# Optimization experiments

Hardware: AMD Instinct MI355X
Metric: run time of the kernel (lower is better)

## Reference

```python
import jax, jax.numpy as jnp
import numpy as np

TEMPERATURE = 0.07
EPS = 1e-12  # F.normalize eps


def _construct_labels(visual_ids, anchor_idx):
    # Faithful vectorization of the original order-dependent double loop:
    # for i < B-1: final write to labels[i] comes from pair (i, B-1)
    #   -> 1 iff ids[i]==anchor_id and ids[B-1]==anchor_id, else 0
    # for i == B-1: final write comes from pair (B-2, B-1)
    #   -> 1 iff ids[B-1]==anchor_id and ids[B-2]==anchor_id, else 0
    B = visual_ids.shape[0]
    anchor_id = visual_ids[anchor_idx]
    same = visual_ids == anchor_id  # [B] bool
    labels = jnp.where(same & same[B - 1], 1, 0).astype(jnp.int32)
    labels = labels.at[B - 1].set((same[B - 1] & same[B - 2]).astype(jnp.int32))
    return labels


def setup_inputs() -> dict:
    key = jax.random.key(0)
    k1, k2 = jax.random.split(key)
    visual_feat = jax.random.normal(k1, (8192, 512), dtype=jnp.float32)
    visual_ids = jax.random.randint(k2, (8192,), 0, 1024, dtype=jnp.int64 if jax.config.jax_enable_x64 else jnp.int32)
    anchor_idx = 3
    return {"visual_feat": visual_feat, "visual_ids": visual_ids, "anchor_idx": anchor_idx}


def reference(visual_feat, visual_ids, anchor_idx):
    # L2 normalize rows (F.normalize: x / max(||x||, eps))
    norm = jnp.sqrt(jnp.sum(visual_feat * visual_feat, axis=1, keepdims=True))
    f = visual_feat / jnp.maximum(norm, EPS)
    sim = jnp.matmul(f, f.T) / TEMPERATURE  # [B, B]
    labels = _construct_labels(visual_ids, anchor_idx)  # [B] int in {0,1}
    logp = jax.nn.log_softmax(sim, axis=-1)  # [B, B]
    picked = jnp.take_along_axis(logp, labels[:, None], axis=1)[:, 0]
    loss = -jnp.mean(picked)
    return loss
```

## Files before the change

kernel.cpp:

```cpp
#include <hip/hip_runtime.h>


typedef int i32x8 __attribute__((ext_vector_type(8)));
typedef float f32x4 __attribute__((ext_vector_type(4)));

#define B_N 8192
#define D_K 512
#define ROWB 512
#define INVT 14.285714285714286f
#define SCALE_LOG2 20.609929155556622f

#if defined(__has_builtin) && __has_builtin(__builtin_amdgcn_exp2f)
#define FAST_EXP2(x) __builtin_amdgcn_exp2f(x)
#else
#define FAST_EXP2(x) exp2f(x)
#endif

union FragU {
  int4 h[2];
  i32x8 v;
};

static __device__ __forceinline__ void load16_to_lds(const void* g, void* l) {
  __builtin_amdgcn_global_load_lds(
      (const __attribute__((address_space(1))) unsigned int*)g,
      (__attribute__((address_space(3))) unsigned int*)l, 16, 0, 0);
}

__global__ __launch_bounds__(256)
void norm_kernel(const float* __restrict__ x,
                 unsigned char* __restrict__ fQ,
                 float* __restrict__ Z) {
  const int row = blockIdx.x * 4 + (threadIdx.x >> 6);
  const int lane = threadIdx.x & 63;
  const float4* xr = (const float4*)(x + (size_t)row * D_K);
  float4 a = xr[2 * lane];
  float4 b = xr[2 * lane + 1];
  float s = a.x * a.x + a.y * a.y + a.z * a.z + a.w * a.w +
            b.x * b.x + b.y * b.y + b.z * b.z + b.w * b.w;
#pragma unroll
  for (int off = 1; off < 64; off <<= 1) s += __shfl_xor(s, off);
  const float inv = 1.0f / fmaxf(sqrtf(s), 1e-12f);
  int lo = 0, hi = 0;
  lo = __builtin_amdgcn_cvt_pk_fp8_f32(a.x * inv, a.y * inv, lo, false);
  lo = __builtin_amdgcn_cvt_pk_fp8_f32(a.z * inv, a.w * inv, lo, true);
  hi = __builtin_amdgcn_cvt_pk_fp8_f32(b.x * inv, b.y * inv, hi, false);
  hi = __builtin_amdgcn_cvt_pk_fp8_f32(b.z * inv, b.w * inv, hi, true);
  int2 p; p.x = lo; p.y = hi;
  ((int2*)(fQ + (size_t)row * ROWB))[lane] = p;
  if (lane == 0) Z[row] = 0.0f;
}

__global__ __launch_bounds__(256, 2)
void sim_kernel(const unsigned char* __restrict__ fQ,
                float* __restrict__ Z, float* __restrict__ T01,
                float* __restrict__ D) {
  __shared__ unsigned char ldsA[4][128 * 128];
  __shared__ unsigned char ldsB[128 * 128];

  const int tid = threadIdx.x;
  const int lane = tid & 63;
  const int w = tid >> 6;
  const int wm = w & 1;
  const int wn = w >> 1;
  const int bx = blockIdx.x, by = blockIdx.y;
  const int b = by & 7;
  const int I = (by < 8) ? bx : (63 - bx);
  const int Jfirst = I + ((b - I) & 7);
  if (Jfirst > 63) return;
  const int I0 = I * 128;

  const int srow = lane >> 3;
  const int sb = lane & 7;
  const int su = sb ^ srow;
  const int sg = 2 * (su & 3) + (su >> 2);
  const size_t sOff = (size_t)srow * ROWB + sg * 16;

  const int fr = lane & 15;
  const int q = lane >> 4;
  const int swz = fr & 7;

  const int raRow = (wm * 64 + fr) * 128;
  const unsigned char* rbBase = ldsB + (wn * 64 + fr) * 128;
  const int off0 = (q ^ swz) * 16;
  const int off1 = ((q + 4) ^ swz) * 16;

#pragma unroll
  for (int kk = 0; kk < 4; ++kk) {
    const unsigned char* gA = fQ + (size_t)(I0 + w * 32) * ROWB + kk * 128 + sOff;
    unsigned char* lA = ldsA[kk] + (w * 32) * 128;
#pragma unroll
    for (int rr = 0; rr < 32; rr += 8)
      load16_to_lds(gA + (size_t)rr * ROWB, lA + rr * 128);
  }

  float Zp[4][4];
#pragma unroll
  for (int m = 0; m < 4; ++m)
#pragma unroll
    for (int r = 0; r < 4; ++r) Zp[m][r] = 0.0f;

#pragma unroll 1
  for (int J = Jfirst; J < 64; J += 8) {
    const int J0 = J * 128;
    f32x4 acc[4][4];
#pragma unroll
    for (int m = 0; m < 4; ++m)
#pragma unroll
      for (int n = 0; n < 4; ++n) acc[m][n] = (f32x4){0.f, 0.f, 0.f, 0.f};

#pragma unroll 1
    for (int kk = 0; kk < 4; ++kk) {
      const int k0 = kk * 128;
      {
        const unsigned char* gB = fQ + (size_t)(J0 + w * 32) * ROWB + k0 + sOff;
        unsigned char* lB = ldsB + (w * 32) * 128;
#pragma unroll
        for (int rr = 0; rr < 32; rr += 8)
          load16_to_lds(gB + (size_t)rr * ROWB, lB + rr * 128);
      }
      __syncthreads();

      const unsigned char* raBase = ldsA[kk] + raRow;
      i32x8 bv[4];
#pragma unroll
      for (int n = 0; n < 4; ++n) {
        const unsigned char* rb = rbBase + n * 16 * 128;
        FragU u;
        u.h[0] = *(const int4*)(rb + off0);
        u.h[1] = *(const int4*)(rb + off1);
        bv[n] = u.v;
      }
#pragma unroll
      for (int mh = 0; mh < 2; ++mh) {
        i32x8 av[2];
#pragma unroll
        for (int m = 0; m < 2; ++m) {
          const unsigned char* ra = raBase + (mh * 2 + m) * 16 * 128;
          FragU u;
          u.h[0] = *(const int4*)(ra + off0);
          u.h[1] = *(const int4*)(ra + off1);
          av[m] = u.v;
        }
#pragma unroll
        for (int m = 0; m < 2; ++m)
#pragma unroll
          for (int n = 0; n < 4; ++n)
            acc[mh * 2 + m][n] = __builtin_amdgcn_mfma_scale_f32_16x16x128_f8f6f4(
                av[m], bv[n], acc[mh * 2 + m][n], 0, 0, 0, 127, 0, 127);
      }
      __syncthreads();
    }

    if (I == 0 && wm == 0) {
      if (q == 0) {
#pragma unroll
        for (int n = 0; n < 4; ++n) {
          const int col = J0 + wn * 64 + n * 16 + fr;
          T01[col * 2 + 0] = acc[0][n][0] * INVT;
          T01[col * 2 + 1] = acc[0][n][1] * INVT;
        }
      }
    }

    if (J == I) {
#pragma unroll
      for (int m = 0; m < 4; ++m)
#pragma unroll
        for (int n = 0; n < 4; ++n) {
          const int col = J0 + wn * 64 + n * 16 + fr;
#pragma unroll
          for (int r = 0; r < 4; ++r) {
            const int row = I0 + wm * 64 + m * 16 + q * 4 + r;
            if (row == col) D[row] = acc[m][n][r];
          }
        }
    }

    const bool offd = (J != I);
#pragma unroll
    for (int n = 0; n < 4; ++n) {
      float cs = 0.0f;
#pragma unroll
      for (int m = 0; m < 4; ++m)
#pragma unroll
        for (int r = 0; r < 4; ++r) {
          const float e = FAST_EXP2((acc[m][n][r] - 1.0f) * SCALE_LOG2);
          Zp[m][r] += e;
          cs += e;
        }
      if (offd) {
        cs += __shfl_xor(cs, 16);
        cs += __shfl_xor(cs, 32);
        if (q == 0) atomicAdd(&Z[J0 + wn * 64 + n * 16 + fr], cs);
      }
    }
  }

#pragma unroll
  for (int m = 0; m < 4; ++m)
#pragma unroll
    for (int r = 0; r < 4; ++r) {
      float v = Zp[m][r];
      v += __shfl_xor(v, 1);
      v += __shfl_xor(v, 2);
      v += __shfl_xor(v, 4);
      v += __shfl_xor(v, 8);
      if (fr == 0) atomicAdd(&Z[I0 + wm * 64 + m * 16 + q * 4 + r], v);
    }
}

__global__ __launch_bounds__(1024)
void finalize_kernel(const float* __restrict__ Z,
                     const float* __restrict__ T01,
                     const float* __restrict__ D,
                     const int* __restrict__ ids,
                     const int* __restrict__ anchor,
                     float* __restrict__ out) {
  __shared__ float red[1024];
  const int t = threadIdx.x;
  const int anchor_id = ids[anchor[0]];
  const int sameLast = (ids[B_N - 1] == anchor_id);
  const int samePrev = (ids[B_N - 2] == anchor_id);
  int i[8], id[8];
  float z[8], d[8], t0[8], t1[8];
#pragma unroll
  for (int u = 0; u < 8; ++u) {
    i[u] = u * 1024 + t;
    z[u] = Z[i[u]];
    d[u] = D[i[u]];
    t0[u] = T01[i[u] * 2 + 0];
    t1[u] = T01[i[u] * 2 + 1];
    id[u] = ids[i[u]];
  }
  float sum = 0.0f;
#pragma unroll
  for (int u = 0; u < 8; ++u) {
    const int same_i = (id[u] == anchor_id);
    const int lab =
        (i[u] < B_N - 1) ? (same_i & sameLast) : (sameLast & samePrev);
    const float tt = lab ? t1[u] : t0[u];
    const float Zc = z[u] - FAST_EXP2((d[u] - 1.0f) * SCALE_LOG2) + 1.0f;
    sum += tt - (INVT + logf(Zc));
  }
  red[t] = sum;
  __syncthreads();
  for (int off = 512; off > 0; off >>= 1) {
    if (t < off) red[t] += red[t + off];
    __syncthreads();
  }
  if (t == 0) out[0] = -red[0] / (float)B_N;
}

extern "C" void kernel_launch(void* const* d_in, const int* in_sizes, int n_in,
                              void* d_out, int out_size, void* d_ws, size_t ws_size,
                              hipStream_t stream) {
  const float* x = (const float*)d_in[0];
  const int* ids = (const int*)d_in[1];
  const int* anchor = (const int*)d_in[2];
  float* out = (float*)d_out;

  unsigned char* fQ = (unsigned char*)d_ws;
  float* Z = (float*)((char*)d_ws + (size_t)B_N * ROWB);
  float* T01 = Z + B_N;
  float* D = T01 + 2 * B_N;

  norm_kernel<<<B_N / 4, 256, 0, stream>>>(x, fQ, Z);
  sim_kernel<<<dim3(32, 16), 256, 0, stream>>>(fQ, Z, T01, D);
  finalize_kernel<<<1, 1024, 0, stream>>>(Z, T01, D, ids, anchor, out);
}
```

Baseline: 104.0 us.

## Double-buffer B tiles in LDS and keep last A k-slice in registers

The sim kernel now double-buffers the B tile in LDS, prefetching the next k-slice (or the next J tile's first slice) while MFMAs run on the current one. Full __syncthreads are replaced by explicit vmcnt waits and raw barriers, and MFMA sections get raised wave priority. The fourth A k-slice is held in registers so LDS stays at 5 tiles, which lets two blocks per CU fit. This trades more registers and fragile manual waitcnt ordering for hiding global-to-LDS latency.

```diff
diff --git a/kernel.cpp b/kernel.cpp
--- a/kernel.cpp
+++ b/kernel.cpp
@@ -26,6 +26,16 @@
       (const __attribute__((address_space(1))) unsigned int*)g,
       (__attribute__((address_space(3))) unsigned int*)l, 16, 0, 0);
 }
+
+static __device__ __forceinline__ void bar_nodrain() {
+  __builtin_amdgcn_sched_barrier(0);
+  asm volatile("" ::: "memory");
+  __builtin_amdgcn_s_barrier();
+  asm volatile("" ::: "memory");
+  __builtin_amdgcn_sched_barrier(0);
+}
+
+#define VM_WAIT(N) asm volatile("s_waitcnt vmcnt(" #N ")" ::: "memory")
 
 __global__ __launch_bounds__(256)
 void norm_kernel(const float* __restrict__ x,
@@ -55,8 +65,8 @@
 void sim_kernel(const unsigned char* __restrict__ fQ,
                 float* __restrict__ Z, float* __restrict__ T01,
                 float* __restrict__ D) {
-  __shared__ unsigned char ldsA[4][128 * 128];
-  __shared__ unsigned char ldsB[128 * 128];
+  __shared__ unsigned char ldsA[3 * 128 * 128];
+  __shared__ unsigned char ldsB[2 * 128 * 128];
 
   const int tid = threadIdx.x;
   const int lane = tid & 63;
@@ -81,47 +91,74 @@
   const int swz = fr & 7;
 
   const int raRow = (wm * 64 + fr) * 128;
-  const unsigned char* rbBase = ldsB + (wn * 64 + fr) * 128;
+  const int rbRow = (wn * 64 + fr) * 128;
   const int off0 = (q ^ swz) * 16;
   const int off1 = ((q + 4) ^ swz) * 16;
 
-#pragma unroll
-  for (int kk = 0; kk < 4; ++kk) {
+  FragU u3[4];
+  {
+    const unsigned char* aReg =
+        fQ + (size_t)(I0 + wm * 64 + fr) * ROWB + 3 * 128 + q * 32;
+#pragma unroll
+    for (int m = 0; m < 4; ++m) {
+      const unsigned char* p = aReg + (size_t)(m * 16) * ROWB;
+      u3[m].h[0] = *(const int4*)(p);
+      u3[m].h[1] = *(const int4*)(p + 16);
+    }
+  }
+#pragma unroll
+  for (int m = 0; m < 4; ++m) asm volatile("" ::"v"(u3[m].v));
+
+#pragma unroll
+  for (int kk = 0; kk < 3; ++kk) {
     const unsigned char* gA = fQ + (size_t)(I0 + w * 32) * ROWB + kk * 128 + sOff;
-    unsigned char* lA = ldsA[kk] + (w * 32) * 128;
+    unsigned char* lA = ldsA + kk * (128 * 128) + (w * 32) * 128;
 #pragma unroll
     for (int rr = 0; rr < 32; rr += 8)
       load16_to_lds(gA + (size_t)rr * ROWB, lA + rr * 128);
   }
 
+  int curOff = 0;
+  {
+    const unsigned char* gB =
+        fQ + (size_t)(Jfirst * 128 + w * 32) * ROWB + sOff;
+    unsigned char* lB = ldsB + (w * 32) * 128;
+#pragma unroll
+    for (int rr = 0; rr < 32; rr += 8)
+      load16_to_lds(gB + (size_t)rr * ROWB, lB + rr * 128);
+  }
+
   float Zp[4][4];
 #pragma unroll
   for (int m = 0; m < 4; ++m)
 #pragma unroll
     for (int r = 0; r < 4; ++r) Zp[m][r] = 0.0f;
+
+  f32x4 acc[4][4];
 
 #pragma unroll 1
   for (int J = Jfirst; J < 64; J += 8) {
     const int J0 = J * 128;
-    f32x4 acc[4][4];
 #pragma unroll
     for (int m = 0; m < 4; ++m)
 #pragma unroll
       for (int n = 0; n < 4; ++n) acc[m][n] = (f32x4){0.f, 0.f, 0.f, 0.f};
 
 #pragma unroll 1
-    for (int kk = 0; kk < 4; ++kk) {
-      const int k0 = kk * 128;
+    for (int kk = 0; kk < 3; ++kk) {
       {
-        const unsigned char* gB = fQ + (size_t)(J0 + w * 32) * ROWB + k0 + sOff;
-        unsigned char* lB = ldsB + (w * 32) * 128;
+        const unsigned char* gB =
+            fQ + (size_t)(J0 + w * 32) * ROWB + (kk + 1) * 128 + sOff;
+        unsigned char* lB = ldsB + (curOff ^ 16384) + (w * 32) * 128;
 #pragma unroll
         for (int rr = 0; rr < 32; rr += 8)
           load16_to_lds(gB + (size_t)rr * ROWB, lB + rr * 128);
       }
-      __syncthreads();
-
-      const unsigned char* raBase = ldsA[kk] + raRow;
+      VM_WAIT(4);
+      bar_nodrain();
+
+      const unsigned char* raBase = ldsA + kk * (128 * 128) + raRow;
+      const unsigned char* rbBase = ldsB + curOff + rbRow;
       i32x8 bv[4];
 #pragma unroll
       for (int n = 0; n < 4; ++n) {
@@ -131,6 +168,7 @@
         u.h[1] = *(const int4*)(rb + off1);
         bv[n] = u.v;
       }
+      __builtin_amdgcn_s_setprio(1);
 #pragma unroll
       for (int mh = 0; mh < 2; ++mh) {
         i32x8 av[2];
@@ -149,8 +187,45 @@
             acc[mh * 2 + m][n] = __builtin_amdgcn_mfma_scale_f32_16x16x128_f8f6f4(
                 av[m], bv[n], acc[mh * 2 + m][n], 0, 0, 0, 127, 0, 127);
       }
-      __syncthreads();
-    }
+      __builtin_amdgcn_s_setprio(0);
+      bar_nodrain();
+      curOff ^= 16384;
+    }
+
+    const bool hasNext = (J + 8) < 64;
+    if (hasNext) {
+      const unsigned char* gB =
+          fQ + (size_t)((J + 8) * 128 + w * 32) * ROWB + sOff;
+      unsigned char* lB = ldsB + (curOff ^ 16384) + (w * 32) * 128;
+#pragma unroll
+      for (int rr = 0; rr < 32; rr += 8)
+        load16_to_lds(gB + (size_t)rr * ROWB, lB + rr * 128);
+      VM_WAIT(4);
+    } else {
+      VM_WAIT(0);
+    }
+    bar_nodrain();
+    {
+      const unsigned char* rbBase = ldsB + curOff + rbRow;
+      i32x8 bv[4];
+#pragma unroll
+      for (int n = 0; n < 4; ++n) {
+        const unsigned char* rb = rbBase + n * 16 * 128;
+        FragU u;
+        u.h[0] = *(const int4*)(rb + off0);
+        u.h[1] = *(const int4*)(rb + off1);
+        bv[n] = u.v;
+      }
+      __builtin_amdgcn_s_setprio(1);
+#pragma unroll
+      for (int m = 0; m < 4; ++m)
+#pragma unroll
+        for (int n = 0; n < 4; ++n)
+          acc[m][n] = __builtin_amdgcn_mfma_scale_f32_16x16x128_f8f6f4(
+              u3[m].v, bv[n], acc[m][n], 0, 0, 0, 127, 0, 127);
+      __builtin_amdgcn_s_setprio(0);
+    }
+    curOff ^= 16384;
 
     if (I == 0 && wm == 0) {
       if (q == 0) {
@@ -195,6 +270,8 @@
         if (q == 0) atomicAdd(&Z[J0 + wn * 64 + n * 16 + fr], cs);
       }
     }
+
+    bar_nodrain();
   }
 
 #pragma unroll
```

Result: slower. 107.4 us (+3.3%).

## Launch one block per upper-triangular tile and load B fragments from global

Applied to the files above, without the earlier changes.

Replaces the 512-block grid, where each block looped over several J tiles of a row band, with 2080 blocks, each computing a single 128x128 tile of the upper triangle. The mapping uses a triangular-index decode in reverse order. B operands are now read directly from global memory into registers with double buffering instead of staging through LDS, which removes the per-k syncthreads. MFMA sections get raised wave priority. The aim is better load balance and less synchronisation, at the cost of reloading the A band for every tile and uncoalesced direct global B reads.

```diff
diff --git a/kernel.cpp b/kernel.cpp
--- a/kernel.cpp
+++ b/kernel.cpp
@@ -7,6 +7,7 @@
 #define B_N 8192
 #define D_K 512
 #define ROWB 512
+#define NTILE 2080
 #define INVT 14.285714285714286f
 #define SCALE_LOG2 20.609929155556622f
 
@@ -56,19 +57,21 @@
                 float* __restrict__ Z, float* __restrict__ T01,
                 float* __restrict__ D) {
   __shared__ unsigned char ldsA[4][128 * 128];
-  __shared__ unsigned char ldsB[128 * 128];
+
+  const int t = blockIdx.x;
+  const int u = (NTILE - 1) - t;
+  int k = (int)((sqrtf(8.0f * (float)u + 1.0f) - 1.0f) * 0.5f);
+  while ((k + 1) * (k + 2) / 2 <= u) ++k;
+  while (k * (k + 1) / 2 > u) --k;
+  const int I = 63 - k;
+  const int J = 63 - (u - k * (k + 1) / 2);
+  const int I0 = I * 128, J0 = J * 128;
 
   const int tid = threadIdx.x;
   const int lane = tid & 63;
   const int w = tid >> 6;
   const int wm = w & 1;
   const int wn = w >> 1;
-  const int bx = blockIdx.x, by = blockIdx.y;
-  const int b = by & 7;
-  const int I = (by < 8) ? bx : (63 - bx);
-  const int Jfirst = I + ((b - I) & 7);
-  if (Jfirst > 63) return;
-  const int I0 = I * 128;
 
   const int srow = lane >> 3;
   const int sb = lane & 7;
@@ -81,7 +84,6 @@
   const int swz = fr & 7;
 
   const int raRow = (wm * 64 + fr) * 128;
-  const unsigned char* rbBase = ldsB + (wn * 64 + fr) * 128;
   const int off0 = (q ^ swz) * 16;
   const int off1 = ((q + 4) ^ swz) * 16;
 
@@ -94,106 +96,108 @@
       load16_to_lds(gA + (size_t)rr * ROWB, lA + rr * 128);
   }
 
+  const unsigned char* bBase =
+      fQ + (size_t)(J0 + wn * 64 + fr) * ROWB + q * 32;
+
+  f32x4 acc[4][4];
+#pragma unroll
+  for (int m = 0; m < 4; ++m)
+#pragma unroll
+    for (int n = 0; n < 4; ++n) acc[m][n] = (f32x4){0.f, 0.f, 0.f, 0.f};
+
+  FragU b0[4], b1[4];
+#pragma unroll
+  for (int n = 0; n < 4; ++n) {
+    const unsigned char* p = bBase + (size_t)(n * 16) * ROWB;
+    b0[n].h[0] = *(const int4*)(p);
+    b0[n].h[1] = *(const int4*)(p + 16);
+  }
+
+  __syncthreads();
+
+#pragma unroll
+  for (int kk = 0; kk < 4; ++kk) {
+    FragU* bc = (kk & 1) ? b1 : b0;
+    FragU* bn = (kk & 1) ? b0 : b1;
+    if (kk < 3) {
+      const unsigned char* pb = bBase + (kk + 1) * 128;
+#pragma unroll
+      for (int n = 0; n < 4; ++n) {
+        const unsigned char* p = pb + (size_t)(n * 16) * ROWB;
+        bn[n].h[0] = *(const int4*)(p);
+        bn[n].h[1] = *(const int4*)(p + 16);
+      }
+    }
+    const unsigned char* raBase = ldsA[kk] + raRow;
+    __builtin_amdgcn_s_setprio(1);
+#pragma unroll
+    for (int mh = 0; mh < 2; ++mh) {
+      i32x8 av[2];
+#pragma unroll
+      for (int m = 0; m < 2; ++m) {
+        const unsigned char* ra = raBase + (mh * 2 + m) * 16 * 128;
+        FragU u;
+        u.h[0] = *(const int4*)(ra + off0);
+        u.h[1] = *(const int4*)(ra + off1);
+        av[m] = u.v;
+      }
+#pragma unroll
+      for (int m = 0; m < 2; ++m)
+#pragma unroll
+        for (int n = 0; n < 4; ++n)
+          acc[mh * 2 + m][n] = __builtin_amdgcn_mfma_scale_f32_16x16x128_f8f6f4(
+              av[m], bc[n].v, acc[mh * 2 + m][n], 0, 0, 0, 127, 0, 127);
+    }
+    __builtin_amdgcn_s_setprio(0);
+  }
+
+  if (I == 0 && wm == 0) {
+    if (q == 0) {
+#pragma unroll
+      for (int n = 0; n < 4; ++n) {
+        const int col = J0 + wn * 64 + n * 16 + fr;
+        T01[col * 2 + 0] = acc[0][n][0] * INVT;
+        T01[col * 2 + 1] = acc[0][n][1] * INVT;
+      }
+    }
+  }
+
+  if (J == I) {
+#pragma unroll
+    for (int m = 0; m < 4; ++m)
+#pragma unroll
+      for (int n = 0; n < 4; ++n) {
+        const int col = J0 + wn * 64 + n * 16 + fr;
+#pragma unroll
+        for (int r = 0; r < 4; ++r) {
+          const int row = I0 + wm * 64 + m * 16 + q * 4 + r;
+          if (row == col) D[row] = acc[m][n][r];
+        }
+      }
+  }
+
+  const bool offd = (J != I);
   float Zp[4][4];
 #pragma unroll
   for (int m = 0; m < 4; ++m)
 #pragma unroll
     for (int r = 0; r < 4; ++r) Zp[m][r] = 0.0f;
 
-#pragma unroll 1
-  for (int J = Jfirst; J < 64; J += 8) {
-    const int J0 = J * 128;
-    f32x4 acc[4][4];
+#pragma unroll
+  for (int n = 0; n < 4; ++n) {
+    float cs = 0.0f;
 #pragma unroll
     for (int m = 0; m < 4; ++m)
 #pragma unroll
-      for (int n = 0; n < 4; ++n) acc[m][n] = (f32x4){0.f, 0.f, 0.f, 0.f};
-
-#pragma unroll 1
-    for (int kk = 0; kk < 4; ++kk) {
-      const int k0 = kk * 128;
-      {
-        const unsigned char* gB = fQ + (size_t)(J0 + w * 32) * ROWB + k0 + sOff;
-        unsigned char* lB = ldsB + (w * 32) * 128;
-#pragma unroll
-        for (int rr = 0; rr < 32; rr += 8)
-          load16_to_lds(gB + (size_t)rr * ROWB, lB + rr * 128);
-      }
-      __syncthreads();
-
-      const unsigned char* raBase = ldsA[kk] + raRow;
-      i32x8 bv[4];
-#pragma unroll
-      for (int n = 0; n < 4; ++n) {
-        const unsigned char* rb = rbBase + n * 16 * 128;
-        FragU u;
-        u.h[0] = *(const int4*)(rb + off0);
-        u.h[1] = *(const int4*)(rb + off1);
-        bv[n] = u.v;
-      }
-#pragma unroll
-      for (int mh = 0; mh < 2; ++mh) {
-        i32x8 av[2];
-#pragma unroll
-        for (int m = 0; m < 2; ++m) {
-          const unsigned char* ra = raBase + (mh * 2 + m) * 16 * 128;
-          FragU u;
-          u.h[0] = *(const int4*)(ra + off0);
-          u.h[1] = *(const int4*)(ra + off1);
-          av[m] = u.v;
-        }
-#pragma unroll
-        for (int m = 0; m < 2; ++m)
-#pragma unroll
-          for (int n = 0; n < 4; ++n)
-            acc[mh * 2 + m][n] = __builtin_amdgcn_mfma_scale_f32_16x16x128_f8f6f4(
-                av[m], bv[n], acc[mh * 2 + m][n], 0, 0, 0, 127, 0, 127);
-      }
-      __syncthreads();
-    }
-
-    if (I == 0 && wm == 0) {
-      if (q == 0) {
-#pragma unroll
-        for (int n = 0; n < 4; ++n) {
-          const int col = J0 + wn * 64 + n * 16 + fr;
-          T01[col * 2 + 0] = acc[0][n][0] * INVT;
-          T01[col * 2 + 1] = acc[0][n][1] * INVT;
-        }
-      }
-    }
-
-    if (J == I) {
-#pragma unroll
-      for (int m = 0; m < 4; ++m)
-#pragma unroll
-        for (int n = 0; n < 4; ++n) {
-          const int col = J0 + wn * 64 + n * 16 + fr;
-#pragma unroll
-          for (int r = 0; r < 4; ++r) {
-            const int row = I0 + wm * 64 + m * 16 + q * 4 + r;
-            if (row == col) D[row] = acc[m][n][r];
-          }
-        }
-    }
-
-    const bool offd = (J != I);
-#pragma unroll
-    for (int n = 0; n < 4; ++n) {
-      float cs = 0.0f;
-#pragma unroll
-      for (int m = 0; m < 4; ++m)
-#pragma unroll
-        for (int r = 0; r < 4; ++r) {
-          const float e = FAST_EXP2((acc[m][n][r] - 1.0f) * SCALE_LOG2);
-          Zp[m][r] += e;
-          cs += e;
-        }
-      if (offd) {
-        cs += __shfl_xor(cs, 16);
-        cs += __shfl_xor(cs, 32);
-        if (q == 0) atomicAdd(&Z[J0 + wn * 64 + n * 16 + fr], cs);
-      }
+      for (int r = 0; r < 4; ++r) {
+        const float e = FAST_EXP2((acc[m][n][r] - 1.0f) * SCALE_LOG2);
+        Zp[m][r] += e;
+        cs += e;
+      }
+    if (offd) {
+      cs += __shfl_xor(cs, 16);
+      cs += __shfl_xor(cs, 32);
+      if (q == 0) atomicAdd(&Z[J0 + wn * 64 + n * 16 + fr], cs);
     }
   }
 
@@ -266,6 +270,6 @@
   float* D = T01 + 2 * B_N;
 
   norm_kernel<<<B_N / 4, 256, 0, stream>>>(x, fQ, Z);
-  sim_kernel<<<dim3(32, 16), 256, 0, stream>>>(fQ, Z, T01, D);
+  sim_kernel<<<NTILE, 256, 0, stream>>>(fQ, Z, T01, D);
   finalize_kernel<<<1, 1024, 0, stream>>>(Z, T01, D, ids, anchor, out);
 }
```

Result: slower. 137.0 us (+31.7%).

## Double-buffer A tile, raise occupancy, split work finer, parallelize finalize reduction

Applied to the files above, without the earlier changes.

The sim kernel now keeps only two A k-slices in LDS and prefetches the next one alongside each B load, which cuts LDS use so three blocks fit per CU. The grid doubles to 64x16, and each block strides J by 16, so each block does half as many tiles and more blocks run in parallel. The finalize step now runs as 8 blocks that reduce with wave shuffles and combine through an atomic sum plus a last-block ticket, replacing the single-block tree reduction. In exchange, A slices are reloaded from global memory for every J tile, and the final sum becomes order-dependent through float atomics.

```diff
diff --git a/kernel.cpp b/kernel.cpp
--- a/kernel.cpp
+++ b/kernel.cpp
@@ -30,7 +30,9 @@
 __global__ __launch_bounds__(256)
 void norm_kernel(const float* __restrict__ x,
                  unsigned char* __restrict__ fQ,
-                 float* __restrict__ Z) {
+                 float* __restrict__ Z,
+                 float* __restrict__ S,
+                 int* __restrict__ ticket) {
   const int row = blockIdx.x * 4 + (threadIdx.x >> 6);
   const int lane = threadIdx.x & 63;
   const float4* xr = (const float4*)(x + (size_t)row * D_K);
@@ -49,13 +51,17 @@
   int2 p; p.x = lo; p.y = hi;
   ((int2*)(fQ + (size_t)row * ROWB))[lane] = p;
   if (lane == 0) Z[row] = 0.0f;
-}
-
-__global__ __launch_bounds__(256, 2)
+  if (blockIdx.x == 0 && threadIdx.x == 0) {
+    S[0] = 0.0f;
+    ticket[0] = 0;
+  }
+}
+
+__global__ __launch_bounds__(256, 3)
 void sim_kernel(const unsigned char* __restrict__ fQ,
                 float* __restrict__ Z, float* __restrict__ T01,
                 float* __restrict__ D) {
-  __shared__ unsigned char ldsA[4][128 * 128];
+  __shared__ unsigned char ldsA[2][128 * 128];
   __shared__ unsigned char ldsB[128 * 128];
 
   const int tid = threadIdx.x;
@@ -64,9 +70,8 @@
   const int wm = w & 1;
   const int wn = w >> 1;
   const int bx = blockIdx.x, by = blockIdx.y;
-  const int b = by & 7;
-  const int I = (by < 8) ? bx : (63 - bx);
-  const int Jfirst = I + ((b - I) & 7);
+  const int I = (by & 1) ? (63 - bx) : bx;
+  const int Jfirst = I + ((by - I) & 15);
   if (Jfirst > 63) return;
   const int I0 = I * 128;
 
@@ -85,10 +90,9 @@
   const int off0 = (q ^ swz) * 16;
   const int off1 = ((q + 4) ^ swz) * 16;
 
-#pragma unroll
-  for (int kk = 0; kk < 4; ++kk) {
-    const unsigned char* gA = fQ + (size_t)(I0 + w * 32) * ROWB + kk * 128 + sOff;
-    unsigned char* lA = ldsA[kk] + (w * 32) * 128;
+  {
+    const unsigned char* gA = fQ + (size_t)(I0 + w * 32) * ROWB + sOff;
+    unsigned char* lA = ldsA[0] + (w * 32) * 128;
 #pragma unroll
     for (int rr = 0; rr < 32; rr += 8)
       load16_to_lds(gA + (size_t)rr * ROWB, lA + rr * 128);
@@ -101,7 +105,7 @@
     for (int r = 0; r < 4; ++r) Zp[m][r] = 0.0f;
 
 #pragma unroll 1
-  for (int J = Jfirst; J < 64; J += 8) {
+  for (int J = Jfirst; J < 64; J += 16) {
     const int J0 = J * 128;
     f32x4 acc[4][4];
 #pragma unroll
@@ -109,19 +113,28 @@
 #pragma unroll
       for (int n = 0; n < 4; ++n) acc[m][n] = (f32x4){0.f, 0.f, 0.f, 0.f};
 
-#pragma unroll 1
+#pragma unroll
     for (int kk = 0; kk < 4; ++kk) {
-      const int k0 = kk * 128;
       {
-        const unsigned char* gB = fQ + (size_t)(J0 + w * 32) * ROWB + k0 + sOff;
+        const unsigned char* gB =
+            fQ + (size_t)(J0 + w * 32) * ROWB + kk * 128 + sOff;
         unsigned char* lB = ldsB + (w * 32) * 128;
 #pragma unroll
         for (int rr = 0; rr < 32; rr += 8)
           load16_to_lds(gB + (size_t)rr * ROWB, lB + rr * 128);
       }
+      {
+        const int p = (kk + 1) & 3;
+        const unsigned char* gA =
+            fQ + (size_t)(I0 + w * 32) * ROWB + p * 128 + sOff;
+        unsigned char* lA = ldsA[(kk + 1) & 1] + (w * 32) * 128;
+#pragma unroll
+        for (int rr = 0; rr < 32; rr += 8)
+          load16_to_lds(gA + (size_t)rr * ROWB, lA + rr * 128);
+      }
       __syncthreads();
 
-      const unsigned char* raBase = ldsA[kk] + raRow;
+      const unsigned char* raBase = ldsA[kk & 1] + raRow;
       i32x8 bv[4];
 #pragma unroll
       for (int n = 0; n < 4; ++n) {
@@ -216,40 +229,45 @@
                      const float* __restrict__ D,
                      const int* __restrict__ ids,
                      const int* __restrict__ anchor,
+                     float* __restrict__ S,
+                     int* __restrict__ ticket,
                      float* __restrict__ out) {
-  __shared__ float red[1024];
+  __shared__ float red[16];
   const int t = threadIdx.x;
+  const int row = blockIdx.x * 1024 + t;
   const int anchor_id = ids[anchor[0]];
   const int sameLast = (ids[B_N - 1] == anchor_id);
   const int samePrev = (ids[B_N - 2] == anchor_id);
-  int i[8], id[8];
-  float z[8], d[8], t0[8], t1[8];
-#pragma unroll
-  for (int u = 0; u < 8; ++u) {
-    i[u] = u * 1024 + t;
-    z[u] = Z[i[u]];
-    d[u] = D[i[u]];
-    t0[u] = T01[i[u] * 2 + 0];
-    t1[u] = T01[i[u] * 2 + 1];
-    id[u] = ids[i[u]];
-  }
-  float sum = 0.0f;
-#pragma unroll
-  for (int u = 0; u < 8; ++u) {
-    const int same_i = (id[u] == anchor_id);
-    const int lab =
-        (i[u] < B_N - 1) ? (same_i & sameLast) : (sameLast & samePrev);
-    const float tt = lab ? t1[u] : t0[u];
-    const float Zc = z[u] - FAST_EXP2((d[u] - 1.0f) * SCALE_LOG2) + 1.0f;
-    sum += tt - (INVT + logf(Zc));
-  }
-  red[t] = sum;
+  const float z = Z[row];
+  const float d = D[row];
+  const float t0 = T01[row * 2 + 0];
+  const float t1 = T01[row * 2 + 1];
+  const int id = ids[row];
+
+  const int same_i = (id == anchor_id);
+  const int lab = (row < B_N - 1) ? (same_i & sameLast) : (sameLast & samePrev);
+  const float tt = lab ? t1 : t0;
+  const float Zc = z - FAST_EXP2((d - 1.0f) * SCALE_LOG2) + 1.0f;
+  float sum = tt - (INVT + logf(Zc));
+
+#pragma unroll
+  for (int off = 1; off < 64; off <<= 1) sum += __shfl_xor(sum, off);
+  if ((t & 63) == 0) red[t >> 6] = sum;
   __syncthreads();
-  for (int off = 512; off > 0; off >>= 1) {
-    if (t < off) red[t] += red[t + off];
-    __syncthreads();
-  }
-  if (t == 0) out[0] = -red[0] / (float)B_N;
+  if (t < 64) {
+    float v = (t < 16) ? red[t] : 0.0f;
+#pragma unroll
+    for (int off = 1; off < 16; off <<= 1) v += __shfl_xor(v, off);
+    if (t == 0) {
+      atomicAdd(S, v);
+      __threadfence();
+      const int old = atomicAdd(ticket, 1);
+      if (old == 7) {
+        const float tot = atomicAdd(S, 0.0f);
+        out[0] = -tot / (float)B_N;
+      }
+    }
+  }
 }
 
 extern "C" void kernel_launch(void* const* d_in, const int* in_sizes, int n_in,
@@ -264,8 +282,10 @@
   float* Z = (float*)((char*)d_ws + (size_t)B_N * ROWB);
   float* T01 = Z + B_N;
   float* D = T01 + 2 * B_N;
-
-  norm_kernel<<<B_N / 4, 256, 0, stream>>>(x, fQ, Z);
-  sim_kernel<<<dim3(32, 16), 256, 0, stream>>>(fQ, Z, T01, D);
-  finalize_kernel<<<1, 1024, 0, stream>>>(Z, T01, D, ids, anchor, out);
-}
+  float* S = D + B_N;
+  int* ticket = (int*)(S + 1);
+
+  norm_kernel<<<B_N / 4, 256, 0, stream>>>(x, fQ, Z, S, ticket);
+  sim_kernel<<<dim3(64, 16), 256, 0, stream>>>(fQ, Z, T01, D);
+  finalize_kernel<<<8, 1024, 0, stream>>>(Z, T01, D, ids, anchor, S, ticket, out);
+}
```

Result: slower. 344.0 us (+230.9%).
